# Optimization experiments

Measured on AMD Instinct MI355X. Metric: run time of the kernel, lower is better.

Reference implementation:

```python
import jax, jax.numpy as jnp
import numpy as np

B, H, S, D = 2, 16, 2048, 64

def setup_inputs() -> dict:
    key = jax.random.key(0)
    kq, kk, kv = jax.random.split(key, 3)
    q = jax.random.normal(kq, (B, H, S, D), dtype=jnp.float32)
    k = jax.random.normal(kk, (B, H, S, D), dtype=jnp.float32)
    v = jax.random.normal(kv, (B, H, S, D), dtype=jnp.float32)
    return {"q": q, "k": k, "v": v}

def reference(q, k, v):
    d_k = q.shape[-1]
    scale = 1.0 / jnp.sqrt(jnp.asarray(d_k, dtype=q.dtype))
    # scores: [B, H, Sq, Sk]
    scores = jnp.einsum("bhqd,bhkd->bhqk", q, k) * scale
    attn = jax.nn.softmax(scores, axis=-1)
    out = jnp.einsum("bhqk,bhkd->bhqd", attn, v)
    return out
```

## Files before the change

### kernel.cpp

```cpp
#include <hip/hip_runtime.h>
#include <math.h>

constexpr int Bc = 2, Hc = 16, Sc = 2048, Dc = 64;
constexpr int BQ = 64;
constexpr int BK = 32;
constexpr int NT = Sc / BK;

constexpr int KWD = 36;
constexpr int VWD = 21;

typedef __attribute__((ext_vector_type(8))) short short8v;
typedef __attribute__((ext_vector_type(4))) float f32x4;
typedef __attribute__((ext_vector_type(4))) unsigned int uint4v;

__device__ __forceinline__ unsigned int cvt_pk_bf16(float lo, float hi) {
    unsigned int d;
    asm("v_cvt_pk_bf16_f32 %0, %1, %2" : "=v"(d) : "v"(lo), "v"(hi));
    return d;
}

__global__ __launch_bounds__(256, 4)
void attn_mfma_kernel(const float* __restrict__ Q,
                      const float* __restrict__ K,
                      const float* __restrict__ V,
                      float* __restrict__ O)
{
    __shared__ __align__(16) unsigned int Ksd[2][32 * KWD];
    __shared__ __align__(16) unsigned int Vtd[2][64 * VWD];

    const int tid  = threadIdx.x;
    const int wave = tid >> 6;
    const int lane = tid & 63;
    const int n    = lane & 15;
    const int qd   = lane >> 4;

    const int hid = blockIdx.x;
    const int hk  = hid >> 3;
    const int bh  = (hid & 7) + 8 * (hk >> 5);
    const int q0  = (hk & 31) * BQ;

    const float* Qg = Q + ((size_t)bh * Sc + q0) * Dc;
    const float* Kg = K + (size_t)bh * Sc * Dc;
    const float* Vg = V + (size_t)bh * Sc * Dc;
    float*       Og = O + ((size_t)bh * Sc + q0) * Dc;

    short8v q_frag[2];
#pragma unroll
    for (int kc = 0; kc < 2; ++kc) {
        const float* qrow = Qg + (wave * 16 + n) * Dc + kc * 32 + qd * 8;
        float4 f0 = *reinterpret_cast<const float4*>(qrow);
        float4 f1 = *reinterpret_cast<const float4*>(qrow + 4);
        uint4v u;
        u[0] = cvt_pk_bf16(f0.x * 0.125f, f0.y * 0.125f);
        u[1] = cvt_pk_bf16(f0.z * 0.125f, f0.w * 0.125f);
        u[2] = cvt_pk_bf16(f1.x * 0.125f, f1.y * 0.125f);
        u[3] = cvt_pk_bf16(f1.z * 0.125f, f1.w * 0.125f);
        q_frag[kc] = __builtin_bit_cast(short8v, u);
    }

    const f32x4 z = {0.f, 0.f, 0.f, 0.f};
    f32x4 o_acc[4] = {z, z, z, z};
    float l_part = 0.f;

    float4 ka, kb;
    float2 va[2], vb[2];
    const int kr2 = tid >> 3;
    const int kc8 = (tid & 7) << 3;
    const int vkp = tid >> 4;
    const int dp0 = tid & 15;

    const float* kbase = Kg + kr2 * Dc + kc8;
    const float* vbase = Vg + vkp * 2 * Dc + dp0 * 2;

    auto load_regs = [&](int kt) {
        const float* Kt = kbase + kt * (BK * Dc);
        const float* Vt = vbase + kt * (BK * Dc);
        ka    = *reinterpret_cast<const float4*>(Kt);
        kb    = *reinterpret_cast<const float4*>(Kt + 4);
        va[0] = *reinterpret_cast<const float2*>(Vt);
        vb[0] = *reinterpret_cast<const float2*>(Vt + Dc);
        va[1] = *reinterpret_cast<const float2*>(Vt + 32);
        vb[1] = *reinterpret_cast<const float2*>(Vt + Dc + 32);
    };
    auto write_lds = [&](int bb) {
        uint4v w;
        w[0] = cvt_pk_bf16(ka.x, ka.y);
        w[1] = cvt_pk_bf16(ka.z, ka.w);
        w[2] = cvt_pk_bf16(kb.x, kb.y);
        w[3] = cvt_pk_bf16(kb.z, kb.w);
        *reinterpret_cast<uint4v*>(&Ksd[bb][kr2 * KWD + (tid & 7) * 4]) = w;
        unsigned int* vd = &Vtd[bb][0];
        vd[(dp0 * 2)            * VWD + vkp] = cvt_pk_bf16(va[0].x, vb[0].x);
        vd[(dp0 * 2 + 1)        * VWD + vkp] = cvt_pk_bf16(va[0].y, vb[0].y);
        vd[((dp0 + 16) * 2)     * VWD + vkp] = cvt_pk_bf16(va[1].x, vb[1].x);
        vd[((dp0 + 16) * 2 + 1) * VWD + vkp] = cvt_pk_bf16(va[1].y, vb[1].y);
    };

    load_regs(0);
    write_lds(0);
    __syncthreads();

    int cur = 0;
    for (int kt = 0; kt < NT; ++kt) {
        const bool more = (kt + 1 < NT);
        if (more) load_regs(kt + 1);

        f32x4 st[2] = {z, z};
        __builtin_amdgcn_s_setprio(1);
#pragma unroll
        for (int nt = 0; nt < 2; ++nt)
#pragma unroll
            for (int kc = 0; kc < 2; ++kc) {
                short8v kf = *reinterpret_cast<const short8v*>(
                    &Ksd[cur][(nt * 16 + n) * KWD + kc * 16 + qd * 4]);
                st[nt] = __builtin_amdgcn_mfma_f32_16x16x32_bf16(
                    kf, q_frag[kc], st[nt], 0, 0, 0);
            }
        __builtin_amdgcn_s_setprio(0);

        float p00 = __expf(st[0][0]), p01 = __expf(st[0][1]);
        float p02 = __expf(st[0][2]), p03 = __expf(st[0][3]);
        float p10 = __expf(st[1][0]), p11 = __expf(st[1][1]);
        float p12 = __expf(st[1][2]), p13 = __expf(st[1][3]);
        l_part += ((p00 + p01) + (p02 + p03)) + ((p10 + p11) + (p12 + p13));

        unsigned int x0 = cvt_pk_bf16(p00, p01);
        unsigned int x1 = cvt_pk_bf16(p02, p03);
        unsigned int y0 = cvt_pk_bf16(p10, p11);
        unsigned int y1 = cvt_pk_bf16(p12, p13);
        asm("v_permlane32_swap_b32 %0, %1" : "+v"(x0), "+v"(y0));
        asm("v_permlane16_swap_b32 %0, %1" : "+v"(x0), "+v"(y0));
        asm("v_permlane32_swap_b32 %0, %1" : "+v"(x1), "+v"(y1));
        asm("v_permlane16_swap_b32 %0, %1" : "+v"(x1), "+v"(y1));
        uint4v pu; pu[0] = x0; pu[1] = x1; pu[2] = y0; pu[3] = y1;
        short8v p_frag = __builtin_bit_cast(short8v, pu);

        const unsigned int* vt = &Vtd[cur][0];
        __builtin_amdgcn_s_setprio(1);
#pragma unroll
        for (int dt = 0; dt < 4; ++dt) {
            const unsigned int* vrow = vt + (dt * 16 + n) * VWD + qd * 4;
            uint4v vu;
            vu[0] = vrow[0]; vu[1] = vrow[1]; vu[2] = vrow[2]; vu[3] = vrow[3];
            short8v vf = __builtin_bit_cast(short8v, vu);
            o_acc[dt] = __builtin_amdgcn_mfma_f32_16x16x32_bf16(
                p_frag, vf, o_acc[dt], 0, 0, 0);
        }
        __builtin_amdgcn_s_setprio(0);

        if (more) write_lds(cur ^ 1);
        __syncthreads();
        cur ^= 1;
    }

    l_part += __shfl_xor(l_part, 16, 64);
    l_part += __shfl_xor(l_part, 32, 64);
#pragma unroll
    for (int r = 0; r < 4; ++r) {
        float lr  = __shfl(l_part, qd * 4 + r, 64);
        float inv = 1.0f / lr;
#pragma unroll
        for (int dt = 0; dt < 4; ++dt) {
            Og[(wave * 16 + qd * 4 + r) * Dc + dt * 16 + n] = o_acc[dt][r] * inv;
        }
    }
}

extern "C" void kernel_launch(void* const* d_in, const int* in_sizes, int n_in,
                              void* d_out, int out_size, void* d_ws, size_t ws_size,
                              hipStream_t stream) {
    const float* q = (const float*)d_in[0];
    const float* k = (const float*)d_in[1];
    const float* v = (const float*)d_in[2];
    float*       o = (float*)d_out;

    dim3 grid((Sc / BQ) * Bc * Hc);
    attn_mfma_kernel<<<grid, 256, 0, stream>>>(q, k, v, o);
}
```

Measured before the change: 150.1 us.

## Double query tile per block so each wave reuses K/V fragments across two row tiles

Raises the query block from 64 to 128 rows, so each wave now handles two 16-row query tiles and reuses every K and V LDS fragment for two MFMAs. This halves the number of blocks, and with it the global K/V loads, conversions and LDS staging per query row. In exchange it uses more registers (launch bounds lowered to 2 blocks per CU) and gives 512 blocks in the grid, which lowers occupancy and latency hiding.

```diff
diff --git a/kernel.cpp b/kernel.cpp
--- a/kernel.cpp
+++ b/kernel.cpp
@@ -2,7 +2,7 @@
 #include <math.h>
 
 constexpr int Bc = 2, Hc = 16, Sc = 2048, Dc = 64;
-constexpr int BQ = 64;
+constexpr int BQ = 128;
 constexpr int BK = 32;
 constexpr int NT = Sc / BK;
 
@@ -19,7 +19,7 @@
     return d;
 }
 
-__global__ __launch_bounds__(256, 4)
+__global__ __launch_bounds__(256, 2)
 void attn_mfma_kernel(const float* __restrict__ Q,
                       const float* __restrict__ K,
                       const float* __restrict__ V,
@@ -36,31 +36,33 @@
 
     const int hid = blockIdx.x;
     const int hk  = hid >> 3;
-    const int bh  = (hid & 7) + 8 * (hk >> 5);
-    const int q0  = (hk & 31) * BQ;
+    const int bh  = (hid & 7) + 8 * (hk >> 4);
+    const int q0  = (hk & 15) * BQ;
 
     const float* Qg = Q + ((size_t)bh * Sc + q0) * Dc;
     const float* Kg = K + (size_t)bh * Sc * Dc;
     const float* Vg = V + (size_t)bh * Sc * Dc;
     float*       Og = O + ((size_t)bh * Sc + q0) * Dc;
 
-    short8v q_frag[2];
+    short8v q_frag[2][2];
 #pragma unroll
-    for (int kc = 0; kc < 2; ++kc) {
-        const float* qrow = Qg + (wave * 16 + n) * Dc + kc * 32 + qd * 8;
-        float4 f0 = *reinterpret_cast<const float4*>(qrow);
-        float4 f1 = *reinterpret_cast<const float4*>(qrow + 4);
-        uint4v u;
-        u[0] = cvt_pk_bf16(f0.x * 0.125f, f0.y * 0.125f);
-        u[1] = cvt_pk_bf16(f0.z * 0.125f, f0.w * 0.125f);
-        u[2] = cvt_pk_bf16(f1.x * 0.125f, f1.y * 0.125f);
-        u[3] = cvt_pk_bf16(f1.z * 0.125f, f1.w * 0.125f);
-        q_frag[kc] = __builtin_bit_cast(short8v, u);
-    }
+    for (int qt = 0; qt < 2; ++qt)
+#pragma unroll
+        for (int kc = 0; kc < 2; ++kc) {
+            const float* qrow = Qg + (wave * 32 + qt * 16 + n) * Dc + kc * 32 + qd * 8;
+            float4 f0 = *reinterpret_cast<const float4*>(qrow);
+            float4 f1 = *reinterpret_cast<const float4*>(qrow + 4);
+            uint4v u;
+            u[0] = cvt_pk_bf16(f0.x * 0.125f, f0.y * 0.125f);
+            u[1] = cvt_pk_bf16(f0.z * 0.125f, f0.w * 0.125f);
+            u[2] = cvt_pk_bf16(f1.x * 0.125f, f1.y * 0.125f);
+            u[3] = cvt_pk_bf16(f1.z * 0.125f, f1.w * 0.125f);
+            q_frag[qt][kc] = __builtin_bit_cast(short8v, u);
+        }
 
     const f32x4 z = {0.f, 0.f, 0.f, 0.f};
-    f32x4 o_acc[4] = {z, z, z, z};
-    float l_part = 0.f;
+    f32x4 o_acc[2][4] = {{z, z, z, z}, {z, z, z, z}};
+    float l_part[2] = {0.f, 0.f};
 
     float4 ka, kb;
     float2 va[2], vb[2];
@@ -105,7 +107,7 @@
         const bool more = (kt + 1 < NT);
         if (more) load_regs(kt + 1);
 
-        f32x4 st[2] = {z, z};
+        f32x4 st[2][2] = {{z, z}, {z, z}};
         __builtin_amdgcn_s_setprio(1);
 #pragma unroll
         for (int nt = 0; nt < 2; ++nt)
@@ -113,27 +115,33 @@
             for (int kc = 0; kc < 2; ++kc) {
                 short8v kf = *reinterpret_cast<const short8v*>(
                     &Ksd[cur][(nt * 16 + n) * KWD + kc * 16 + qd * 4]);
-                st[nt] = __builtin_amdgcn_mfma_f32_16x16x32_bf16(
-                    kf, q_frag[kc], st[nt], 0, 0, 0);
+#pragma unroll
+                for (int qt = 0; qt < 2; ++qt)
+                    st[qt][nt] = __builtin_amdgcn_mfma_f32_16x16x32_bf16(
+                        kf, q_frag[qt][kc], st[qt][nt], 0, 0, 0);
             }
         __builtin_amdgcn_s_setprio(0);
 
-        float p00 = __expf(st[0][0]), p01 = __expf(st[0][1]);
-        float p02 = __expf(st[0][2]), p03 = __expf(st[0][3]);
-        float p10 = __expf(st[1][0]), p11 = __expf(st[1][1]);
-        float p12 = __expf(st[1][2]), p13 = __expf(st[1][3]);
-        l_part += ((p00 + p01) + (p02 + p03)) + ((p10 + p11) + (p12 + p13));
+        short8v p_frag[2];
+#pragma unroll
+        for (int qt = 0; qt < 2; ++qt) {
+            float p00 = __expf(st[qt][0][0]), p01 = __expf(st[qt][0][1]);
+            float p02 = __expf(st[qt][0][2]), p03 = __expf(st[qt][0][3]);
+            float p10 = __expf(st[qt][1][0]), p11 = __expf(st[qt][1][1]);
+            float p12 = __expf(st[qt][1][2]), p13 = __expf(st[qt][1][3]);
+            l_part[qt] += ((p00 + p01) + (p02 + p03)) + ((p10 + p11) + (p12 + p13));
 
-        unsigned int x0 = cvt_pk_bf16(p00, p01);
-        unsigned int x1 = cvt_pk_bf16(p02, p03);
-        unsigned int y0 = cvt_pk_bf16(p10, p11);
-        unsigned int y1 = cvt_pk_bf16(p12, p13);
-        asm("v_permlane32_swap_b32 %0, %1" : "+v"(x0), "+v"(y0));
-        asm("v_permlane16_swap_b32 %0, %1" : "+v"(x0), "+v"(y0));
-        asm("v_permlane32_swap_b32 %0, %1" : "+v"(x1), "+v"(y1));
-        asm("v_permlane16_swap_b32 %0, %1" : "+v"(x1), "+v"(y1));
-        uint4v pu; pu[0] = x0; pu[1] = x1; pu[2] = y0; pu[3] = y1;
-        short8v p_frag = __builtin_bit_cast(short8v, pu);
+            unsigned int x0 = cvt_pk_bf16(p00, p01);
+            unsigned int x1 = cvt_pk_bf16(p02, p03);
+            unsigned int y0 = cvt_pk_bf16(p10, p11);
+            unsigned int y1 = cvt_pk_bf16(p12, p13);
+            asm("v_permlane32_swap_b32 %0, %1" : "+v"(x0), "+v"(y0));
+            asm("v_permlane16_swap_b32 %0, %1" : "+v"(x0), "+v"(y0));
+            asm("v_permlane32_swap_b32 %0, %1" : "+v"(x1), "+v"(y1));
+            asm("v_permlane16_swap_b32 %0, %1" : "+v"(x1), "+v"(y1));
+            uint4v pu; pu[0] = x0; pu[1] = x1; pu[2] = y0; pu[3] = y1;
+            p_frag[qt] = __builtin_bit_cast(short8v, pu);
+        }
 
         const unsigned int* vt = &Vtd[cur][0];
         __builtin_amdgcn_s_setprio(1);
@@ -143,8 +151,10 @@
             uint4v vu;
             vu[0] = vrow[0]; vu[1] = vrow[1]; vu[2] = vrow[2]; vu[3] = vrow[3];
             short8v vf = __builtin_bit_cast(short8v, vu);
-            o_acc[dt] = __builtin_amdgcn_mfma_f32_16x16x32_bf16(
-                p_frag, vf, o_acc[dt], 0, 0, 0);
+#pragma unroll
+            for (int qt = 0; qt < 2; ++qt)
+                o_acc[qt][dt] = __builtin_amdgcn_mfma_f32_16x16x32_bf16(
+                    p_frag[qt], vf, o_acc[qt][dt], 0, 0, 0);
         }
         __builtin_amdgcn_s_setprio(0);
 
@@ -153,15 +163,20 @@
         cur ^= 1;
     }
 
-    l_part += __shfl_xor(l_part, 16, 64);
-    l_part += __shfl_xor(l_part, 32, 64);
 #pragma unroll
-    for (int r = 0; r < 4; ++r) {
-        float lr  = __shfl(l_part, qd * 4 + r, 64);
-        float inv = 1.0f / lr;
+    for (int qt = 0; qt < 2; ++qt) {
+        float lp = l_part[qt];
+        lp += __shfl_xor(lp, 16, 64);
+        lp += __shfl_xor(lp, 32, 64);
 #pragma unroll
-        for (int dt = 0; dt < 4; ++dt) {
-            Og[(wave * 16 + qd * 4 + r) * Dc + dt * 16 + n] = o_acc[dt][r] * inv;
+        for (int r = 0; r < 4; ++r) {
+            float lr  = __shfl(lp, qd * 4 + r, 64);
+            float inv = 1.0f / lr;
+#pragma unroll
+            for (int dt = 0; dt < 4; ++dt) {
+                Og[(wave * 32 + qt * 16 + qd * 4 + r) * Dc + dt * 16 + n] =
+                    o_acc[qt][dt][r] * inv;
+            }
         }
     }
 }
```

Measured after the change: 135.5 us. 1.11x faster.
